# Kernel tuning notes

Hardware: AMD Instinct MI355X
Metric: run time of the kernel (lower is better)

Reference implementation:

```python
import jax, jax.numpy as jnp
import numpy as np

B, V, HP, WP = 1, 6, 37, 66
N, CD, CC = HP * WP, 768, 256
BEVH = BEVW = 100
Q = BEVH * BEVW
NH, NP, D, Z = 8, 4, 4, 8
HD = CC // NH
PC = (-51.2, -51.2, -5.0, 51.2, 51.2, 3.0)
SCALE, PT, PL = 0.5775, 0.0, 0.0
H2, W2 = 518, 924
EPS = 1e-6


def setup_inputs() -> dict:
    key = jax.random.key(0)
    ks = jax.random.split(key, 10)
    s = 0.02
    return {
        "last_tokens": jax.random.normal(ks[0], (B, V, N, CD), jnp.float32),
        "lidar2img": jax.random.normal(ks[1], (B, V, 4, 4), jnp.float32),
        "proj_w": jax.random.normal(ks[2], (CC, CD), jnp.float32) * s,
        "bev_query": jax.random.normal(ks[3], (Q, CC), jnp.float32) * s,
        "w_view": jnp.zeros((1, V, 1), jnp.float32),
        "vp_w": jax.random.normal(ks[4], (CC, CC), jnp.float32) * s,
        "vp_b": jnp.zeros((CC,), jnp.float32),
        "so_w": jax.random.normal(ks[5], (NH * NP * 2, CC), jnp.float32) * s,
        "so_b": jnp.zeros((NH * NP * 2,), jnp.float32),
        "aw_w": jax.random.normal(ks[6], (NH * NP, CC), jnp.float32) * s,
        "aw_b": jnp.zeros((NH * NP,), jnp.float32),
        "op_w": jax.random.normal(ks[7], (CC, CC), jnp.float32) * s,
        "op_b": jnp.zeros((CC,), jnp.float32),
    }


def _ref_points_3d():
    # normalized pillar reference points, (D, Q, 3) in xyz order, Q = h*BEVW + w
    xs = (jnp.arange(BEVW, dtype=jnp.float32) + 0.5) / BEVW
    ys = (jnp.arange(BEVH, dtype=jnp.float32) + 0.5) / BEVH
    zs = jnp.linspace(0.5, Z - 0.5, D, dtype=jnp.float32) / Z
    gx = jnp.broadcast_to(xs[None, :], (BEVH, BEVW)).reshape(-1)
    gy = jnp.broadcast_to(ys[:, None], (BEVH, BEVW)).reshape(-1)
    return jnp.stack([jnp.broadcast_to(gx, (D, Q)),
                      jnp.broadcast_to(gy, (D, Q)),
                      jnp.broadcast_to(zs[:, None], (D, Q))], axis=-1)


def reference(last_tokens, lidar2img, proj_w, bev_query, w_view,
              vp_w, vp_b, so_w, so_b, aw_w, aw_b, op_w, op_b):
    BV = B * V
    # ---- project 3D BEV pillar points to camera views ----
    ref = _ref_points_3d()  # (D, Q, 3)
    wx = ref[..., 0] * (PC[3] - PC[0]) + PC[0]
    wy = ref[..., 1] * (PC[4] - PC[1]) + PC[1]
    wz = ref[..., 2] * (PC[5] - PC[2]) + PC[2]
    ref4 = jnp.stack([wx, wy, wz, jnp.ones_like(wx)], axis=-1)  # (D, Q, 4)
    cam = jnp.einsum('bvij,dqj->bvdqi', lidar2img, ref4)  # (B, V, D, Q, 4)
    depth = cam[..., 2]
    bev_mask = depth > 1e-5
    uv = cam[..., :2] / jnp.clip(depth, 1e-5)[..., None]
    u = uv[..., 0] * SCALE + PL
    v = uv[..., 1] * SCALE + PT
    in_img = (u >= 0) & (u <= W2 - 1) & (v >= 0) & (v <= H2 - 1)
    valid = bev_mask & in_img
    refx = jnp.clip(u / max(W2 - 1.0, 1.0), 0.0, 1.0)
    refy = jnp.clip(v / max(H2 - 1.0, 1.0), 0.0, 1.0)
    w = jnp.maximum(valid.astype(jnp.float32), EPS)  # (B, V, D, Q)
    den = jnp.maximum(w.sum(2), EPS)
    rx = (refx * w).sum(2) / den
    ry = (refy * w).sum(2) / den
    ref2d = jnp.stack([rx, ry], axis=-1).reshape(BV, Q, 2)

    # ---- value features: 1x1 conv proj + value_proj ----
    val = jnp.einsum('bvnc,oc->bvno', last_tokens, proj_w).reshape(BV, N, CC)
    val = val @ vp_w.T + vp_b
    val = val.reshape(BV, N, NH, HD)

    # ---- deformable attention (single level) ----
    query = jnp.broadcast_to(bev_query[None], (BV, Q, CC))
    off = (query @ so_w.T + so_b).reshape(BV, Q, NH, NP, 2)
    attn = jax.nn.softmax((query @ aw_w.T + aw_b).reshape(BV, Q, NH, NP), axis=-1)
    normalizer = jnp.array([WP, HP], jnp.float32)
    loc = ref2d[:, :, None, None, :] + off / normalizer  # (BV, Q, NH, NP, 2)

    # bilinear sampling, grid_sample semantics (align_corners=False, zero pad)
    x = loc[..., 0] * WP - 0.5
    y = loc[..., 1] * HP - 0.5
    x0 = jnp.floor(x); y0 = jnp.floor(y)
    fx = x - x0; fy = y - y0
    x0i = x0.astype(jnp.int32); y0i = y0.astype(jnp.int32)
    b_idx = jnp.arange(BV)[:, None, None, None]
    h_idx = jnp.arange(NH)[None, None, :, None]

    def corner(xi, yi, wgt):
        ok = ((xi >= 0) & (xi < WP) & (yi >= 0) & (yi < HP)).astype(val.dtype)
        lin = jnp.clip(yi, 0, HP - 1) * WP + jnp.clip(xi, 0, WP - 1)
        g = val[b_idx, lin, h_idx]  # (BV, Q, NH, NP, HD)
        return g * (ok * wgt)[..., None]

    samp = (corner(x0i, y0i, (1 - fx) * (1 - fy))
            + corner(x0i + 1, y0i, fx * (1 - fy))
            + corner(x0i, y0i + 1, (1 - fx) * fy)
            + corner(x0i + 1, y0i + 1, fx * fy))
    out = (samp * attn[..., None]).sum(3).reshape(BV, Q, CC)
    out = out @ op_w.T + op_b + query  # residual (mmcv identity)

    # ---- view-weighted combine ----
    out = out.reshape(B, V, Q, CC)
    wv = jax.nn.softplus(w_view)  # (1, V, 1)
    num = (out * wv[..., None]).sum(1)  # (B, Q, CC)
    den_v = jnp.maximum(wv.sum(1), EPS)[..., None]
    bev = num / den_v
    return jnp.transpose(bev, (0, 2, 1)).reshape(B, CC, BEVH, BEVW)
```

## Files before the change

### kernel.cpp

```cpp
#include <hip/hip_runtime.h>
#include <math.h>

#define Q_TOT 10000
#define NVIEW 6
#define NTOK  2442
#define HP_   37
#define WP_   66
#define CD_   768
#define CC_   256

typedef __attribute__((ext_vector_type(8))) short bf16x8;
typedef __attribute__((ext_vector_type(4))) float f32x4;

__device__ inline unsigned f2bf(float f) {
    unsigned u = __builtin_bit_cast(unsigned, f);
    unsigned r = u + 0x7FFFu + ((u >> 16) & 1u);
    return r >> 16;
}

__device__ __forceinline__ void glds16(const void* g, void* l) {
    __builtin_amdgcn_global_load_lds(
        (const __attribute__((address_space(1))) unsigned int*)g,
        (__attribute__((address_space(3))) unsigned int*)l,
        16, 0, 0);
}

__global__ __launch_bounds__(256) void prep_all(const float* __restrict__ lt,
                                                const float* __restrict__ vp_w,
                                                const float* __restrict__ proj_w,
                                                const float* __restrict__ opw,
                                                const float* __restrict__ l2i,
                                                const float* __restrict__ so_w,
                                                const float* __restrict__ so_b,
                                                const float* __restrict__ aw_w,
                                                const float* __restrict__ aw_b,
                                                const float* __restrict__ wview,
                                                unsigned short* __restrict__ ltB,
                                                unsigned short* __restrict__ W2b,
                                                unsigned short* __restrict__ opwb,
                                                float* __restrict__ ref2d,
                                                unsigned short* __restrict__ WQb,
                                                float* __restrict__ bqp,
                                                float* __restrict__ vwn) {
    int b0 = blockIdx.x, tid = threadIdx.x;
    if (b0 < 5495) {
        int i = b0 * 256 + tid;
        if (i < 1406592) {
            float4 a = *(const float4*)(lt + (size_t)i * 8);
            float4 c4 = *(const float4*)(lt + (size_t)i * 8 + 4);
            uint4 o;
            o.x = f2bf(a.x) | (f2bf(a.y) << 16);
            o.y = f2bf(a.z) | (f2bf(a.w) << 16);
            o.z = f2bf(c4.x) | (f2bf(c4.y) << 16);
            o.w = f2bf(c4.z) | (f2bf(c4.w) << 16);
            *(uint4*)(ltB + (size_t)i * 8) = o;
        }
        return;
    }
    if (b0 < 6263) {
        int b = b0 - 5495;
        int o2 = b / 3;
        int c = (b % 3) * 256 + tid;
        __shared__ float vps[256];
        vps[tid] = vp_w[(size_t)o2 * 256 + tid];
        __syncthreads();
        float acc = 0.f;
#pragma unroll 16
        for (int o = 0; o < 256; ++o) {
            acc += vps[o] * proj_w[(size_t)o * CD_ + c];
        }
        W2b[(size_t)o2 * CD_ + c] = (unsigned short)f2bf(acc);
        return;
    }
    if (b0 < 6295) {
        int i = (b0 - 6263) * 256 + tid;
        float4 a = *(const float4*)(opw + (size_t)i * 8);
        float4 c4 = *(const float4*)(opw + (size_t)i * 8 + 4);
        uint4 o;
        o.x = f2bf(a.x) | (f2bf(a.y) << 16);
        o.y = f2bf(a.z) | (f2bf(a.w) << 16);
        o.z = f2bf(c4.x) | (f2bf(c4.y) << 16);
        o.w = f2bf(c4.z) | (f2bf(c4.w) << 16);
        *(uint4*)(opwb + (size_t)i * 8) = o;
        return;
    }
    if (b0 < 6530) {
        int idx = (b0 - 6295) * 256 + tid;
        if (idx < NVIEW * Q_TOT) {
            int v = idx / Q_TOT, q = idx % Q_TOT;
            int wq = q % 100, hq = q / 100;
            float wx = (wq + 0.5f) * 1.024f - 51.2f;
            float wy = (hq + 0.5f) * 1.024f - 51.2f;
            const float* L = l2i + v * 16;
            float L0=L[0],L1=L[1],L2=L[2],L3=L[3],L4=L[4],L5=L[5],L6=L[6],L7=L[7];
            float L8=L[8],L9=L[9],L10=L[10],L11=L[11];
            float sw = 0.f, sx = 0.f, sy = 0.f;
#pragma unroll
            for (int d = 0; d < 4; ++d) {
                float zs = (0.5f + (float)d * (7.0f / 3.0f)) * 0.125f;
                float wz = zs * 8.0f - 5.0f;
                float c0 = L0 * wx + L1 * wy + L2 * wz + L3;
                float c1 = L4 * wx + L5 * wy + L6 * wz + L7;
                float c2 = L8 * wx + L9 * wy + L10 * wz + L11;
                bool bm = c2 > 1e-5f;
                float dc = fmaxf(c2, 1e-5f);
                float u  = (c0 / dc) * 0.5775f;
                float vv = (c1 / dc) * 0.5775f;
                bool in_img = (u >= 0.f) && (u <= 923.f) && (vv >= 0.f) && (vv <= 517.f);
                bool valid = bm && in_img;
                float refx = fminf(fmaxf(u / 923.0f, 0.f), 1.f);
                float refy = fminf(fmaxf(vv / 517.0f, 0.f), 1.f);
                float w = valid ? 1.0f : 1e-6f;
                sw += w; sx += refx * w; sy += refy * w;
            }
            float den = fmaxf(sw, 1e-6f);
            ref2d[(size_t)idx * 2 + 0] = sx / den;
            ref2d[(size_t)idx * 2 + 1] = sy / den;
        }
        return;
    }
    {
        int row = b0 - 6530, col = tid;
        float v = (row < 64) ? so_w[row * 256 + col] : (row < 96 ? aw_w[(row - 64) * 256 + col] : 0.f);
        WQb[row * 256 + col] = (unsigned short)f2bf(v);
        if (row == 0 && col < 128) bqp[col] = (col < 64) ? so_b[col] : (col < 96 ? aw_b[col - 64] : 0.f);
        if (row == 1 && col == 0) {
            float sp[6], swv = 0.f;
#pragma unroll
            for (int vv = 0; vv < NVIEW; ++vv) {
                float x = wview[vv];
                float s = (x > 20.f) ? x : log1pf(expf(x));
                sp[vv] = s; swv += s;
            }
            float inv = 1.0f / fmaxf(swv, 1e-6f);
#pragma unroll
            for (int vv = 0; vv < NVIEW; ++vv) vwn[vv] = sp[vv] * inv;
            vwn[6] = swv * inv;
            vwn[7] = 0.f;
        }
    }
}

template <int MODE, int KT>
__device__ __forceinline__ void gemm_glds(char* lds,
                                          const unsigned short* __restrict__ Ah,
                                          const unsigned short* __restrict__ Bw,
                                          const float* __restrict__ bias,
                                          const float* __restrict__ resid,
                                          const float* __restrict__ wview,
                                          void* __restrict__ Cptr,
                                          int M, int nt_shift, int bid, int nwg) {
    constexpr int K = KT * 64;
    int tid = threadIdx.x;
    int wid = tid >> 6, lane = tid & 63;

    int qd = nwg >> 3, r = nwg & 7;
    int xcd = bid & 7, seq = bid >> 3;
    int wgid = (xcd < r) ? (xcd * (qd + 1) + seq) : (r * (qd + 1) + (xcd - r) * qd + seq);
    int mt = wgid >> nt_shift;
    int nt = wgid & ((1 << nt_shift) - 1);
    int m0 = mt * 64, n0 = nt * 64;

    int lr = lane & 15, lq = lane >> 4;
    float* Cf = (float*)Cptr;
    unsigned short* Ch = (unsigned short*)Cptr;

    f32x4 acc[4];
#pragma unroll
    for (int j = 0; j < 4; ++j) acc[j] = (f32x4)(0.f);

#define STAGE(BI, KTI) do {                                                           \
    char* buf = lds + (BI) * 16384;                                                   \
    int k0b = (KTI) << 7;                                                             \
    _Pragma("unroll")                                                                 \
    for (int i_ = 0; i_ < 2; ++i_) {                                                  \
        int L_ = tid + (i_ << 8);                                                     \
        int row_ = L_ >> 3, c_ = L_ & 7;                                              \
        glds16((const char*)Ah + (size_t)(m0 + row_) * (K * 2) + k0b + ((c_ ^ (row_ & 7)) << 4), \
               buf + (L_ << 4));                                                      \
    }                                                                                 \
    _Pragma("unroll")                                                                 \
    for (int i_ = 0; i_ < 2; ++i_) {                                                  \
        int L_ = tid + (i_ << 8);                                                     \
        int row_ = L_ >> 3, c_ = L_ & 7;                                              \
        glds16((const char*)Bw + (size_t)(n0 + row_) * (K * 2) + k0b + ((c_ ^ (row_ & 7)) << 4), \
               buf + 8192 + (L_ << 4));                                               \
    }                                                                                 \
} while (0)

#define GMFMA(BI) do {                                                                \
    char* Abb = lds + (BI) * 16384;                                                   \
    char* Bbb = Abb + 8192;                                                           \
    _Pragma("unroll")                                                                 \
    for (int s_ = 0; s_ < 2; ++s_) {                                                  \
        int chunk_ = (s_ << 2) + lq;                                                  \
        int arow_ = (wid << 4) + lr;                                                  \
        bf16x8 af_ = *(bf16x8*)(Abb + arow_ * 128 + ((chunk_ ^ (arow_ & 7)) << 4));   \
        _Pragma("unroll")                                                             \
        for (int j_ = 0; j_ < 4; ++j_) {                                              \
            int brow_ = (j_ << 4) + lr;                                               \
            bf16x8 bf_ = *(bf16x8*)(Bbb + brow_ * 128 + ((chunk_ ^ (brow_ & 7)) << 4)); \
            acc[j_] = __builtin_amdgcn_mfma_f32_16x16x32_bf16(af_, bf_, acc[j_], 0, 0, 0); \
        }                                                                             \
    }                                                                                 \
} while (0)

    STAGE(0, 0);
    if (KT > 1) STAGE(1, 1);
#pragma unroll
    for (int kt = 0; kt < KT; ++kt) {
        if (kt + 1 < KT) {
            asm volatile("s_waitcnt vmcnt(4)" ::: "memory");
        } else {
            asm volatile("s_waitcnt vmcnt(0)" ::: "memory");
        }
        __builtin_amdgcn_s_barrier();
        __builtin_amdgcn_sched_barrier(0);
        if (kt + 2 < KT) STAGE((kt + 2) % 3, kt + 2);
        GMFMA(kt % 3);
        __builtin_amdgcn_sched_barrier(0);
    }

    int mb = m0 + (wid << 4) + (lq << 2);
    if (MODE == 0) {
#pragma unroll
        for (int j = 0; j < 4; ++j) {
            int n = n0 + (j << 4) + lr;
            float bn = bias[n];
#pragma unroll
            for (int e = 0; e < 4; ++e) {
                int m = mb + e;
                if (m < M) Ch[(size_t)m * 256 + n] = (unsigned short)f2bf(acc[j][e] + bn);
            }
        }
    } else {
        float s = 0.f;
#pragma unroll
        for (int v = 0; v < 6; ++v) {
            float x = wview[v];
            s += (x > 20.f) ? x : log1pf(expf(x));
        }
        float f = s / fmaxf(s, 1e-6f);
#pragma unroll
        for (int j = 0; j < 4; ++j) {
            int n = n0 + (j << 4) + lr;
            float bn = bias[n];
            if (mb + 4 <= M) {
                float4 o;
                float* oo = (float*)&o;
#pragma unroll
                for (int e = 0; e < 4; ++e)
                    oo[e] = acc[j][e] + f * (bn + resid[(size_t)(mb + e) * 256 + n]);
                *(float4*)(Cf + (size_t)n * M + mb) = o;
            } else {
#pragma unroll
                for (int e = 0; e < 4; ++e) {
                    int m = mb + e;
                    if (m < M) Cf[(size_t)n * M + m] = acc[j][e] + f * (bn + resid[(size_t)m * 256 + n]);
                }
            }
        }
    }
#undef STAGE
#undef GMFMA
}

template <int KT>
__device__ __forceinline__ void gemm_f32A(char* base0, char* base1,
                                          const float* __restrict__ Af,
                                          const unsigned short* __restrict__ Bw,
                                          const float* __restrict__ bias,
                                          float* __restrict__ Cf,
                                          int M, int nt_shift, int bid, int nwg) {
    constexpr int K = KT * 64;
    int tid = threadIdx.x;
    int wid = tid >> 6, lane = tid & 63;

    int qd = nwg >> 3, r = nwg & 7;
    int xcd = bid & 7, seq = bid >> 3;
    int wgid = (xcd < r) ? (xcd * (qd + 1) + seq) : (r * (qd + 1) + (xcd - r) * qd + seq);
    int mt = wgid >> nt_shift;
    int nt = wgid & ((1 << nt_shift) - 1);
    int m0 = mt * 64, n0 = nt * 64;

    int lr = lane & 15, lq = lane >> 4;
    int arow_s = tid >> 4;
    int ac4 = tid & 15;

    f32x4 acc[4];
#pragma unroll
    for (int j = 0; j < 4; ++j) acc[j] = (f32x4)(0.f);

    float4 aF[2][4];
    uint4  bR[2][2];
    const float4 zf4 = make_float4(0.f, 0.f, 0.f, 0.f);

#define QLOADG(S, KTI) do {                                                           \
    int k0 = (KTI) << 6;                                                              \
    _Pragma("unroll")                                                                 \
    for (int p_ = 0; p_ < 4; ++p_) {                                                  \
        int row_ = p_ * 16 + arow_s;                                                  \
        bool av_ = (m0 + row_) < M;                                                   \
        aF[S][p_] = av_ ? *(const float4*)(Af + (size_t)(m0 + row_) * K + k0 + ac4 * 4) : zf4; \
    }                                                                                 \
    _Pragma("unroll")                                                                 \
    for (int i_ = 0; i_ < 2; ++i_) {                                                  \
        int s_ = tid + (i_ << 8);                                                     \
        int row_ = s_ >> 3, c_ = s_ & 7;                                              \
        bR[S][i_] = *(const uint4*)(Bw + (size_t)(n0 + row_) * K + k0 + c_ * 8);      \
    }                                                                                 \
} while (0)

#define QTOLDS(S, PB) do {                                                            \
    char* Abb = (PB) ? base1 : base0;                                                 \
    _Pragma("unroll")                                                                 \
    for (int p_ = 0; p_ < 4; ++p_) {                                                  \
        int row_ = p_ * 16 + arow_s;                                                  \
        const float* f_ = (const float*)&aF[S][p_];                                   \
        uint2 w_;                                                                     \
        w_.x = f2bf(f_[0]) | (f2bf(f_[1]) << 16);                                     \
        w_.y = f2bf(f_[2]) | (f2bf(f_[3]) << 16);                                     \
        int byte_ = row_ * 128 + (((ac4 >> 1) ^ (row_ & 7)) << 4) + ((ac4 & 1) << 3); \
        *(uint2*)(Abb + byte_) = w_;                                                  \
    }                                                                                 \
    char* Bbb = Abb + 8192;                                                           \
    _Pragma("unroll")                                                                 \
    for (int i_ = 0; i_ < 2; ++i_) {                                                  \
        int s_ = tid + (i_ << 8);                                                     \
        int row_ = s_ >> 3, c_ = s_ & 7;                                              \
        *(uint4*)(Bbb + row_ * 128 + ((c_ ^ (row_ & 7)) << 4)) = bR[S][i_];           \
    }                                                                                 \
} while (0)

#define QMFMAS(PB) do {                                                               \
    char* Abb = (PB) ? base1 : base0;                                                 \
    char* Bbb = Abb + 8192;                                                           \
    _Pragma("unroll")                                                                 \
    for (int s_ = 0; s_ < 2; ++s_) {                                                  \
        int chunk_ = (s_ << 2) + lq;                                                  \
        int arow_ = (wid << 4) + lr;                                                  \
        bf16x8 af_ = *(bf16x8*)(Abb + arow_ * 128 + ((chunk_ ^ (arow_ & 7)) << 4));   \
        _Pragma("unroll")                                                             \
        for (int j_ = 0; j_ < 4; ++j_) {                                              \
            int brow_ = (j_ << 4) + lr;                                               \
            bf16x8 bf_ = *(bf16x8*)(Bbb + brow_ * 128 + ((chunk_ ^ (brow_ & 7)) << 4)); \
            acc[j_] = __builtin_amdgcn_mfma_f32_16x16x32_bf16(af_, bf_, acc[j_], 0, 0, 0); \
        }                                                                             \
    }                                                                                 \
} while (0)

    QLOADG(0, 0);
#pragma unroll
    for (int kt = 0; kt < KT; ++kt) {
        if (kt + 1 < KT) QLOADG((kt + 1) & 1, kt + 1);
        QTOLDS(kt & 1, kt & 1);
        __builtin_amdgcn_sched_barrier(0);
        asm volatile("s_waitcnt lgkmcnt(0)" ::: "memory");
        __builtin_amdgcn_s_barrier();
        __builtin_amdgcn_sched_barrier(0);
        QMFMAS(kt & 1);
    }

    int mb = m0 + (wid << 4) + (lq << 2);
#pragma unroll
    for (int j = 0; j < 4; ++j) {
        int n = n0 + (j << 4) + lr;
        if (n >= 96) continue;
        float bn = bias[n];
#pragma unroll
        for (int e = 0; e < 4; ++e) {
            int m = mb + e;
            if (m < M) Cf[(size_t)m * 96 + n] = acc[j][e] + bn;
        }
    }
#undef QLOADG
#undef QTOLDS
#undef QMFMAS
}

__global__ __launch_bounds__(256, 3) void dual_gemm(const unsigned short* __restrict__ ltB,
                                                    const unsigned short* __restrict__ W2b,
                                                    const float* __restrict__ vpb,
                                                    unsigned short* __restrict__ valB,
                                                    const float* __restrict__ bqq,
                                                    const unsigned short* __restrict__ WQb,
                                                    const float* __restrict__ bqp,
                                                    float* __restrict__ qout) {
    __shared__ char lds[49152];
    if (blockIdx.x < 916)
        gemm_glds<0, 12>(lds, ltB, W2b, vpb, nullptr, nullptr,
                         (void*)valB, 14652, 2, blockIdx.x, 916);
    else
        gemm_f32A<4>(lds, lds + 16384, bqq, WQb, bqp, qout, Q_TOT, 1, blockIdx.x - 916, 314);
}

__global__ __launch_bounds__(256, 3) void out_gemm(const unsigned short* __restrict__ sampavgB,
                                                   const unsigned short* __restrict__ opwb,
                                                   const float* __restrict__ opb,
                                                   const float* __restrict__ bqq,
                                                   const float* __restrict__ wview,
                                                   float* __restrict__ out) {
    __shared__ char lds[49152];
    gemm_glds<1, 4>(lds, sampavgB, opwb, opb, bqq, wview,
                    (void*)out, Q_TOT, 2, blockIdx.x, gridDim.x);
}

__global__ __launch_bounds__(256) void sample_kernel(const unsigned short* __restrict__ valB,
                                                     const float* __restrict__ ref2d,
                                                     const float* __restrict__ qout,
                                                     const float* __restrict__ vwn,
                                                     unsigned short* __restrict__ sampavgB) {
    __shared__ uint4  sOff[4 * 240];
    __shared__ float4 sW[4 * 240];
    __shared__ float4 sAt[4 * 8];
    __shared__ float  sVw[8];
    int tid = threadIdx.x;
    int qb = blockIdx.x * 4;

    if (tid < 32) {
        int ql = tid >> 3, h = tid & 7;
        const float* qo = qout + (size_t)(qb + ql) * 96 + 64 + h * 4;
        float a0 = qo[0], a1 = qo[1], a2 = qo[2], a3 = qo[3];
        float mx = fmaxf(fmaxf(a0, a1), fmaxf(a2, a3));
        float e0 = __expf(a0 - mx), e1 = __expf(a1 - mx), e2 = __expf(a2 - mx), e3 = __expf(a3 - mx);
        float inv = 1.0f / (e0 + e1 + e2 + e3);
        sAt[ql * 8 + h] = make_float4(e0 * inv, e1 * inv, e2 * inv, e3 * inv);
        if (tid < 8) sVw[tid] = vwn[tid < 6 ? tid : 0];
    }
    __syncthreads();

#pragma unroll
    for (int t = tid; t < 768; t += 256) {
        int ql = t / 192;
        int rem = t - ql * 192;
        int v = rem >> 5;
        int h = (rem >> 2) & 7;
        int p = rem & 3;
        int q = qb + ql;
        const float* qo = qout + (size_t)q * 96;
        float ox = qo[h * 8 + 2 * p];
        float oy = qo[h * 8 + 2 * p + 1];
        float at = ((const float*)&sAt[ql * 8 + h])[p];
        float scale = at * sVw[v];

        float rx = ref2d[(size_t)(v * Q_TOT + q) * 2 + 0];
        float ry = ref2d[(size_t)(v * Q_TOT + q) * 2 + 1];
        float x = rx * 66.0f + ox - 0.5f;
        float y = ry * 37.0f + oy - 0.5f;
        float xf = floorf(x), yf = floorf(y);
        float fx = x - xf, fy = y - yf;
        int xi = (int)xf, yi = (int)yf;

        float cw[4] = { (1.f - fx) * (1.f - fy), fx * (1.f - fy), (1.f - fx) * fy, fx * fy };
        unsigned off[4];
#pragma unroll
        for (int cyi = 0; cyi < 2; ++cyi) {
#pragma unroll
            for (int cxi = 0; cxi < 2; ++cxi) {
                int cx = xi + cxi, cy = yi + cyi;
                bool ok = (cx >= 0) && (cx < WP_) && (cy >= 0) && (cy < HP_);
                int ccx = cx < 0 ? 0 : (cx > WP_ - 1 ? WP_ - 1 : cx);
                int ccy = cy < 0 ? 0 : (cy > HP_ - 1 ? HP_ - 1 : cy);
                int c_ = cyi * 2 + cxi;
                off[c_] = (unsigned)((v * NTOK + ccy * WP_ + ccx) << 9);
                cw[c_] = ok ? cw[c_] * scale : 0.f;
            }
        }
        int slot = ql * 240 + v * 40 + h * 5 + p;
        sOff[slot] = make_uint4(off[0], off[1], off[2], off[3]);
        sW[slot]   = make_float4(cw[0], cw[1], cw[2], cw[3]);
    }
    __syncthreads();

    int ql = tid >> 6;
    int lane = tid & 63;
    int h = lane >> 3, d4 = (lane & 7) << 2;
    unsigned coff = (unsigned)((h * 32 + d4) << 1);
    const char* vbase = (const char*)valB;
    float acc0 = 0.f, acc1 = 0.f, acc2 = 0.f, acc3 = 0.f;
#pragma unroll
    for (int v = 0; v < NVIEW; ++v) {
#pragma unroll
        for (int p = 0; p < 4; ++p) {
            int slot = ql * 240 + v * 40 + h * 5 + p;
            uint4 off = sOff[slot];
            float4 w = sW[slot];
            uint2 r0 = *(const uint2*)(vbase + (off.x + coff));
            uint2 r1 = *(const uint2*)(vbase + (off.y + coff));
            uint2 r2 = *(const uint2*)(vbase + (off.z + coff));
            uint2 r3 = *(const uint2*)(vbase + (off.w + coff));
            float g0, g1;
            g0 = __builtin_bit_cast(float, r0.x << 16); g1 = __builtin_bit_cast(float, r0.x & 0xFFFF0000u);
            acc0 += w.x * g0; acc1 += w.x * g1;
            g0 = __builtin_bit_cast(float, r0.y << 16); g1 = __builtin_bit_cast(float, r0.y & 0xFFFF0000u);
            acc2 += w.x * g0; acc3 += w.x * g1;
            g0 = __builtin_bit_cast(float, r1.x << 16); g1 = __builtin_bit_cast(float, r1.x & 0xFFFF0000u);
            acc0 += w.y * g0; acc1 += w.y * g1;
            g0 = __builtin_bit_cast(float, r1.y << 16); g1 = __builtin_bit_cast(float, r1.y & 0xFFFF0000u);
            acc2 += w.y * g0; acc3 += w.y * g1;
            g0 = __builtin_bit_cast(float, r2.x << 16); g1 = __builtin_bit_cast(float, r2.x & 0xFFFF0000u);
            acc0 += w.z * g0; acc1 += w.z * g1;
            g0 = __builtin_bit_cast(float, r2.y << 16); g1 = __builtin_bit_cast(float, r2.y & 0xFFFF0000u);
            acc2 += w.z * g0; acc3 += w.z * g1;
            g0 = __builtin_bit_cast(float, r3.x << 16); g1 = __builtin_bit_cast(float, r3.x & 0xFFFF0000u);
            acc0 += w.w * g0; acc1 += w.w * g1;
            g0 = __builtin_bit_cast(float, r3.y << 16); g1 = __builtin_bit_cast(float, r3.y & 0xFFFF0000u);
            acc2 += w.w * g0; acc3 += w.w * g1;
        }
    }
    int q = qb + ql;
    unsigned u0 = f2bf(acc0) | (f2bf(acc1) << 16);
    unsigned u1 = f2bf(acc2) | (f2bf(acc3) << 16);
    *(uint2*)(sampavgB + (size_t)q * CC_ + h * 32 + d4) = make_uint2(u0, u1);
}

extern "C" void kernel_launch(void* const* d_in, const int* in_sizes, int n_in,
                              void* d_out, int out_size, void* d_ws, size_t ws_size,
                              hipStream_t stream) {
    const float* lt   = (const float*)d_in[0];
    const float* l2i  = (const float*)d_in[1];
    const float* proj = (const float*)d_in[2];
    const float* bqq  = (const float*)d_in[3];
    const float* wv   = (const float*)d_in[4];
    const float* vpw  = (const float*)d_in[5];
    const float* vpb  = (const float*)d_in[6];
    const float* sow  = (const float*)d_in[7];
    const float* sob  = (const float*)d_in[8];
    const float* aww  = (const float*)d_in[9];
    const float* awb  = (const float*)d_in[10];
    const float* opw  = (const float*)d_in[11];
    const float* opb  = (const float*)d_in[12];
    float* out = (float*)d_out;

    char* ws = (char*)d_ws;
    unsigned short* W2b   = (unsigned short*)(ws);
    unsigned short* opwb  = (unsigned short*)(ws + 393216);
    unsigned short* WQb   = (unsigned short*)(ws + 524288);
    float*          bqp   = (float*)(ws + 589824);
    float*          vwn   = (float*)(ws + 590336);
    float*          ref2d = (float*)(ws + 590848);
    float*          qout  = (float*)(ws + 1070848);
    unsigned short* valB  = (unsigned short*)(ws + 4910848);
    unsigned short* ltB   = (unsigned short*)(ws + 12412672);
    unsigned short* sampavgB = (unsigned short*)(ws + 12412672);

    hipLaunchKernelGGL(prep_all, dim3(6658), dim3(256), 0, stream,
                       lt, vpw, proj, opw, l2i, sow, sob, aww, awb, wv,
                       ltB, W2b, opwb, ref2d, WQb, bqp, vwn);
    hipLaunchKernelGGL(dual_gemm, dim3(1230), dim3(256), 0, stream,
                       ltB, W2b, vpb, valB, bqq, WQb, bqp, qout);
    hipLaunchKernelGGL(sample_kernel, dim3(Q_TOT / 4), dim3(256), 0, stream,
                       valB, ref2d, qout, vwn, sampavgB);
    hipLaunchKernelGGL(out_gemm, dim3(628), dim3(256), 0, stream,
                       sampavgB, opwb, opb, bqq, wv, out);
}
```

Before: 92.87 us.

## Fuse fp32-to-bf16 token conversion into value-projection GEMM A-tile loads

```diff
diff --git a/kernel.cpp b/kernel.cpp
--- a/kernel.cpp
+++ b/kernel.cpp
@@ -25,8 +25,7 @@
         16, 0, 0);
 }
 
-__global__ __launch_bounds__(256) void prep_all(const float* __restrict__ lt,
-                                                const float* __restrict__ vp_w,
+__global__ __launch_bounds__(256) void prep_all(const float* __restrict__ vp_w,
                                                 const float* __restrict__ proj_w,
                                                 const float* __restrict__ opw,
                                                 const float* __restrict__ l2i,
@@ -35,7 +34,6 @@
                                                 const float* __restrict__ aw_w,
                                                 const float* __restrict__ aw_b,
                                                 const float* __restrict__ wview,
-                                                unsigned short* __restrict__ ltB,
                                                 unsigned short* __restrict__ W2b,
                                                 unsigned short* __restrict__ opwb,
                                                 float* __restrict__ ref2d,
@@ -43,24 +41,9 @@
                                                 float* __restrict__ bqp,
                                                 float* __restrict__ vwn) {
     int b0 = blockIdx.x, tid = threadIdx.x;
-    if (b0 < 5495) {
-        int i = b0 * 256 + tid;
-        if (i < 1406592) {
-            float4 a = *(const float4*)(lt + (size_t)i * 8);
-            float4 c4 = *(const float4*)(lt + (size_t)i * 8 + 4);
-            uint4 o;
-            o.x = f2bf(a.x) | (f2bf(a.y) << 16);
-            o.y = f2bf(a.z) | (f2bf(a.w) << 16);
-            o.z = f2bf(c4.x) | (f2bf(c4.y) << 16);
-            o.w = f2bf(c4.z) | (f2bf(c4.w) << 16);
-            *(uint4*)(ltB + (size_t)i * 8) = o;
-        }
-        return;
-    }
-    if (b0 < 6263) {
-        int b = b0 - 5495;
-        int o2 = b / 3;
-        int c = (b % 3) * 256 + tid;
+    if (b0 < 768) {
+        int o2 = b0 / 3;
+        int c = (b0 % 3) * 256 + tid;
         __shared__ float vps[256];
         vps[tid] = vp_w[(size_t)o2 * 256 + tid];
         __syncthreads();
@@ -72,8 +55,9 @@
         W2b[(size_t)o2 * CD_ + c] = (unsigned short)f2bf(acc);
         return;
     }
-    if (b0 < 6295) {
-        int i = (b0 - 6263) * 256 + tid;
+    int b = b0 - 768;
+    if (b < 32) {
+        int i = b * 256 + tid;
         float4 a = *(const float4*)(opw + (size_t)i * 8);
         float4 c4 = *(const float4*)(opw + (size_t)i * 8 + 4);
         uint4 o;
@@ -82,10 +66,8 @@
         o.z = f2bf(c4.x) | (f2bf(c4.y) << 16);
         o.w = f2bf(c4.z) | (f2bf(c4.w) << 16);
         *(uint4*)(opwb + (size_t)i * 8) = o;
-        return;
-    }
-    if (b0 < 6530) {
-        int idx = (b0 - 6295) * 256 + tid;
+    } else if (b < 267) {
+        int idx = (b - 32) * 256 + tid;
         if (idx < NVIEW * Q_TOT) {
             int v = idx / Q_TOT, q = idx % Q_TOT;
             int wq = q % 100, hq = q / 100;
@@ -117,10 +99,8 @@
             ref2d[(size_t)idx * 2 + 0] = sx / den;
             ref2d[(size_t)idx * 2 + 1] = sy / den;
         }
-        return;
-    }
-    {
-        int row = b0 - 6530, col = tid;
+    } else {
+        int row = b - 267, col = tid;
         float v = (row < 64) ? so_w[row * 256 + col] : (row < 96 ? aw_w[(row - 64) * 256 + col] : 0.f);
         WQb[row * 256 + col] = (unsigned short)f2bf(v);
         if (row == 0 && col < 128) bqp[col] = (col < 64) ? so_b[col] : (col < 96 ? aw_b[col - 64] : 0.f);
@@ -139,6 +119,106 @@
             vwn[7] = 0.f;
         }
     }
+}
+
+template <int KT>
+__device__ __forceinline__ void gemm_glds32A(char* lds,
+                                             const float* __restrict__ Af,
+                                             const unsigned short* __restrict__ Bw,
+                                             const float* __restrict__ bias,
+                                             unsigned short* __restrict__ Ch,
+                                             int M, int bid, int nwg) {
+    constexpr int K = KT * 64;
+    int tid = threadIdx.x;
+    int wid = tid >> 6, lane = tid & 63;
+
+    int qd = nwg >> 3, r = nwg & 7;
+    int xcd = bid & 7, seq = bid >> 3;
+    int wgid = (xcd < r) ? (xcd * (qd + 1) + seq) : (r * (qd + 1) + (xcd - r) * qd + seq);
+    int mt = wgid >> 2;
+    int nt = wgid & 3;
+    int m0 = mt * 64, n0 = nt * 64;
+
+    int lr = lane & 15, lq = lane >> 4;
+
+    f32x4 acc[4];
+#pragma unroll
+    for (int j = 0; j < 4; ++j) acc[j] = (f32x4)(0.f);
+
+#define STAGE(BI, KTI) do {                                                           \
+    char* bufA = lds + (BI) * 24576;                                                  \
+    char* bufB = bufA + 16384;                                                        \
+    _Pragma("unroll")                                                                 \
+    for (int i_ = 0; i_ < 4; ++i_) {                                                  \
+        int L_ = tid + (i_ << 8);                                                     \
+        int row_ = L_ >> 4, ch_ = L_ & 15;                                            \
+        int gr_ = m0 + row_; gr_ = gr_ < M ? gr_ : M - 1;                             \
+        glds16((const char*)Af + (size_t)gr_ * (K * 4) + ((KTI) << 8) + ((ch_ ^ (row_ & 7)) << 4), \
+               bufA + (L_ << 4));                                                     \
+    }                                                                                 \
+    _Pragma("unroll")                                                                 \
+    for (int i_ = 0; i_ < 2; ++i_) {                                                  \
+        int L_ = tid + (i_ << 8);                                                     \
+        int row_ = L_ >> 3, c_ = L_ & 7;                                              \
+        glds16((const char*)Bw + (size_t)(n0 + row_) * (K * 2) + ((KTI) << 7) + ((c_ ^ (row_ & 7)) << 4), \
+               bufB + (L_ << 4));                                                     \
+    }                                                                                 \
+} while (0)
+
+#define GMFMA(BI) do {                                                                \
+    char* bufA = lds + (BI) * 24576;                                                  \
+    char* bufB = bufA + 16384;                                                        \
+    _Pragma("unroll")                                                                 \
+    for (int s_ = 0; s_ < 2; ++s_) {                                                  \
+        int cg_ = (s_ << 2) + lq;                                                     \
+        int arow_ = (wid << 4) + lr;                                                  \
+        f32x4 a0_ = *(f32x4*)(bufA + arow_ * 256 + ((((cg_ << 1))     ^ (arow_ & 7)) << 4)); \
+        f32x4 a1_ = *(f32x4*)(bufA + arow_ * 256 + ((((cg_ << 1) | 1) ^ (arow_ & 7)) << 4)); \
+        unsigned w0_, w1_, w2_, w3_;                                                  \
+        asm("v_cvt_pk_bf16_f32 %0, %1, %2" : "=v"(w0_) : "v"(a0_[0]), "v"(a0_[1]));   \
+        asm("v_cvt_pk_bf16_f32 %0, %1, %2" : "=v"(w1_) : "v"(a0_[2]), "v"(a0_[3]));   \
+        asm("v_cvt_pk_bf16_f32 %0, %1, %2" : "=v"(w2_) : "v"(a1_[0]), "v"(a1_[1]));   \
+        asm("v_cvt_pk_bf16_f32 %0, %1, %2" : "=v"(w3_) : "v"(a1_[2]), "v"(a1_[3]));   \
+        bf16x8 af_ = __builtin_bit_cast(bf16x8, make_uint4(w0_, w1_, w2_, w3_));      \
+        _Pragma("unroll")                                                             \
+        for (int j_ = 0; j_ < 4; ++j_) {                                              \
+            int brow_ = (j_ << 4) + lr;                                               \
+            bf16x8 bf_ = *(bf16x8*)(bufB + brow_ * 128 + ((cg_ ^ (brow_ & 7)) << 4)); \
+            acc[j_] = __builtin_amdgcn_mfma_f32_16x16x32_bf16(af_, bf_, acc[j_], 0, 0, 0); \
+        }                                                                             \
+    }                                                                                 \
+} while (0)
+
+    STAGE(0, 0);
+    if (KT > 1) STAGE(1, 1);
+#pragma unroll
+    for (int kt = 0; kt < KT; ++kt) {
+        if (kt + 1 < KT) {
+            asm volatile("s_waitcnt vmcnt(6)" ::: "memory");
+        } else {
+            asm volatile("s_waitcnt vmcnt(0)" ::: "memory");
+        }
+        __builtin_amdgcn_s_barrier();
+        __builtin_amdgcn_sched_barrier(0);
+        GMFMA(kt & 1);
+        __builtin_amdgcn_sched_barrier(0);
+        __builtin_amdgcn_s_barrier();
+        if (kt + 2 < KT) STAGE(kt & 1, kt + 2);
+    }
+
+    int mb = m0 + (wid << 4) + (lq << 2);
+#pragma unroll
+    for (int j = 0; j < 4; ++j) {
+        int n = n0 + (j << 4) + lr;
+        float bn = bias[n];
+#pragma unroll
+        for (int e = 0; e < 4; ++e) {
+            int m = mb + e;
+            if (m < M) Ch[(size_t)m * 256 + n] = (unsigned short)f2bf(acc[j][e] + bn);
+        }
+    }
+#undef STAGE
+#undef GMFMA
 }
 
 template <int MODE, int KT>
@@ -163,7 +243,6 @@
 
     int lr = lane & 15, lq = lane >> 4;
     float* Cf = (float*)Cptr;
-    unsigned short* Ch = (unsigned short*)Cptr;
 
     f32x4 acc[4];
 #pragma unroll
@@ -221,19 +300,7 @@
         __builtin_amdgcn_sched_barrier(0);
     }
 
-    int mb = m0 + (wid << 4) + (lq << 2);
-    if (MODE == 0) {
-#pragma unroll
-        for (int j = 0; j < 4; ++j) {
-            int n = n0 + (j << 4) + lr;
-            float bn = bias[n];
-#pragma unroll
-            for (int e = 0; e < 4; ++e) {
-                int m = mb + e;
-                if (m < M) Ch[(size_t)m * 256 + n] = (unsigned short)f2bf(acc[j][e] + bn);
-            }
-        }
-    } else {
+    {
         float s = 0.f;
 #pragma unroll
         for (int v = 0; v < 6; ++v) {
@@ -241,6 +308,7 @@
             s += (x > 20.f) ? x : log1pf(expf(x));
         }
         float f = s / fmaxf(s, 1e-6f);
+        int mb = m0 + (wid << 4) + (lq << 2);
 #pragma unroll
         for (int j = 0; j < 4; ++j) {
             int n = n0 + (j << 4) + lr;
@@ -378,7 +446,7 @@
 #undef QMFMAS
 }
 
-__global__ __launch_bounds__(256, 3) void dual_gemm(const unsigned short* __restrict__ ltB,
+__global__ __launch_bounds__(256, 3) void dual_gemm(const float* __restrict__ lt,
                                                     const unsigned short* __restrict__ W2b,
                                                     const float* __restrict__ vpb,
                                                     unsigned short* __restrict__ valB,
@@ -388,8 +456,7 @@
                                                     float* __restrict__ qout) {
     __shared__ char lds[49152];
     if (blockIdx.x < 916)
-        gemm_glds<0, 12>(lds, ltB, W2b, vpb, nullptr, nullptr,
-                         (void*)valB, 14652, 2, blockIdx.x, 916);
+        gemm_glds32A<12>(lds, lt, W2b, vpb, valB, 14652, blockIdx.x, 916);
     else
         gemm_f32A<4>(lds, lds + 16384, bqq, WQb, bqp, qout, Q_TOT, 1, blockIdx.x - 916, 314);
 }
@@ -541,14 +608,13 @@
     float*          ref2d = (float*)(ws + 590848);
     float*          qout  = (float*)(ws + 1070848);
     unsigned short* valB  = (unsigned short*)(ws + 4910848);
-    unsigned short* ltB   = (unsigned short*)(ws + 12412672);
     unsigned short* sampavgB = (unsigned short*)(ws + 12412672);
 
-    hipLaunchKernelGGL(prep_all, dim3(6658), dim3(256), 0, stream,
-                       lt, vpw, proj, opw, l2i, sow, sob, aww, awb, wv,
-                       ltB, W2b, opwb, ref2d, WQb, bqp, vwn);
+    hipLaunchKernelGGL(prep_all, dim3(1163), dim3(256), 0, stream,
+                       vpw, proj, opw, l2i, sow, sob, aww, awb, wv,
+                       W2b, opwb, ref2d, WQb, bqp, vwn);
     hipLaunchKernelGGL(dual_gemm, dim3(1230), dim3(256), 0, stream,
-                       ltB, W2b, vpb, valB, bqq, WQb, bqp, qout);
+                       lt, W2b, vpb, valB, bqq, WQb, bqp, qout);
     hipLaunchKernelGGL(sample_kernel, dim3(Q_TOT / 4), dim3(256), 0, stream,
                        valB, ref2d, qout, vwn, sampavgB);
     hipLaunchKernelGGL(out_gemm, dim3(628), dim3(256), 0, stream,
```

Measured after the change: 78.80 us (median of 2 runs). -15.2%, faster.
